# Kernel optimization log

Hardware: AMD Instinct MI355X
Metric: run time of the kernel (lower is better)

## Reference

```python
import jax, jax.numpy as jnp
import numpy as np

NUM_ITERS = 3

def squash(s, axis=-1):
    # standard capsule squash: ||s||^2/(1+||s||^2) * s/||s||
    sq = jnp.sum(s * s, axis=axis, keepdims=True)
    norm = jnp.sqrt(sq)
    return (sq / (1.0 + sq)) * (s / norm)

def setup_inputs() -> dict:
    key = jax.random.key(0)
    kx, kw = jax.random.split(key)
    B, I, k, l, O = 512, 1152, 8, 16, 7
    x = jax.random.normal(kx, (B, I, k), dtype=jnp.float32)
    w = jax.random.normal(kw, (I, k, l, O), dtype=jnp.float32)
    return {"x": x, "w": w}

def reference(x, w):
    # x: [B, I, k]; w: [I, k, l, O]
    u_hat = jnp.einsum('BIk,IklO->BIlO', x, w)            # [B, I, l, O]
    I, _, l, _ = w.shape
    b_ij = jnp.zeros((I, l), dtype=u_hat.dtype)
    v_j = None
    for _ in range(NUM_ITERS):
        c_ij = jax.nn.softmax(b_ij, axis=0)               # softmax over I
        s_j = jnp.einsum('Il,BIlO->BlO', c_ij, u_hat)     # [B, l, O]
        v_j = jnp.transpose(squash(s_j), (0, 2, 1))       # [B, O, l]
        u_vj = jnp.einsum('BOl,BIlO->BIl', v_j, u_hat).mean(axis=0)  # [I, l]
        b_ij = b_ij + u_vj
    return v_j
```

## Files before the change

### kernel.cpp

```cpp
#include <hip/hip_runtime.h>
#include <hip/hip_bf16.h>


#define NB 512
#define NI 1152
#define NLO 112
#define NIK 9216
#define NPAD 128

typedef __attribute__((ext_vector_type(8))) short bf16x8;
typedef __attribute__((ext_vector_type(4))) float f32x4;

__device__ __forceinline__ ushort f2bf(float f) {
    __hip_bfloat16 h = __float2bfloat16(f);
    return *(ushort*)&h;
}
__device__ __forceinline__ float bf2f(short s) {
    union { unsigned int u; float f; } v;
    v.u = ((unsigned int)(unsigned short)s) << 16;
    return v.f;
}

__device__ __forceinline__ void conv_x_body(const float* __restrict__ x,
                                            ushort* __restrict__ xbf,
                                            ushort* __restrict__ xT, int bid) {
    __shared__ ushort tile[64][68];
    int kg = bid % 144, bg = bid / 144;
    int k0 = kg * 64, b0 = bg * 64;
    int t = threadIdx.x;
    for (int e = t; e < 1024; e += 256) {
        int r = e >> 4, c4 = (e & 15) * 4;
        float4 f = *(const float4*)&x[(size_t)(b0 + r) * NIK + k0 + c4];
        ushort4 u = { f2bf(f.x), f2bf(f.y), f2bf(f.z), f2bf(f.w) };
        *(ushort4*)&xbf[(size_t)(b0 + r) * NIK + k0 + c4] = u;
        tile[r][c4] = u.x; tile[r][c4 + 1] = u.y; tile[r][c4 + 2] = u.z; tile[r][c4 + 3] = u.w;
    }
    __syncthreads();
    for (int e = t; e < 1024; e += 256) {
        int kr = e >> 4, c4 = (e & 15) * 4;
        ushort4 u = { tile[c4][kr], tile[c4 + 1][kr], tile[c4 + 2][kr], tile[c4 + 3][kr] };
        *(ushort4*)&xT[(size_t)(k0 + kr) * NB + b0 + c4] = u;
    }
}

__global__ __launch_bounds__(256) void prep0(const float* __restrict__ x,
                                             ushort* __restrict__ xbf,
                                             ushort* __restrict__ xT,
                                             const float* __restrict__ w,
                                             ushort* __restrict__ wpT,
                                             float* __restrict__ eb,
                                             float* __restrict__ Z) {
    if (blockIdx.x < 1152) { conv_x_body(x, xbf, xT, blockIdx.x); return; }
    __shared__ ushort tile[NPAD][66];
    int t = threadIdx.x;
    int wb = blockIdx.x - 1152;
    int ik0 = wb * 64;
    if (blockIdx.x == 1152 && t < 48) Z[t] = (t < 16) ? 1152.0f : 0.0f;
    if (t < 128) eb[(size_t)(wb * 8 + (t >> 4)) * 16 + (t & 15)] = 1.0f;
    for (int e = t; e < 8192; e += 256) {
        int ikl = e >> 7, np = e & 127;
        int l = np >> 3, o = np & 7;
        float wv = (o < 7) ? w[(size_t)(ik0 + ikl) * NLO + l * 7 + o] : 0.f;
        tile[np][ikl] = f2bf(wv);
    }
    __syncthreads();
    for (int e = t; e < 8192; e += 256) {
        int np = e >> 6, ikl = e & 63;
        wpT[(size_t)np * NIK + ik0 + ikl] = tile[np][ikl];
    }
}

__global__ __launch_bounds__(1024) void sq_gemm(const ushort* __restrict__ xbf,
                                                const ushort* __restrict__ wpT,
                                                const float* __restrict__ eb,
                                                const float* __restrict__ Zit,
                                                ushort* __restrict__ vT,
                                                float* __restrict__ out, int wout) {
    __shared__ float csl[NI * 2];
    __shared__ float sp[16][16][16];
    __shared__ float ss[16][16];
    __shared__ float facs[16][2];
    __shared__ float zi[2];
    int bid = blockIdx.x;
    int mt = bid & 31, ng = bid >> 5;
    int b0 = mt * 16, n0 = ng * 16;
    int t = threadIdx.x;
    int wv = t >> 6, lane = t & 63;
    int row = lane & 15, quad = lane >> 4;
    int k0 = wv * 576;
    for (int e = t; e < NI * 2; e += 1024) {
        int i = e >> 1, ls = e & 1;
        csl[e] = eb[(size_t)i * 16 + ng * 2 + ls];
    }
    if (t < 2) zi[t] = 1.0f / Zit[ng * 2 + t];
    __syncthreads();
    const ushort* ap = xbf + (size_t)(b0 + row) * NIK + k0 + quad * 8;
    const ushort* bp = wpT + (size_t)(n0 + row) * NIK + k0 + quad * 8;
    int lsel = row >> 3;
    int i0 = (k0 >> 3) + quad;
    f32x4 acc = {0.f, 0.f, 0.f, 0.f};
    #pragma unroll 6
    for (int ks = 0; ks < 18; ++ks) {
        bf16x8 a = *(const bf16x8*)(ap + ks * 32);
        bf16x8 wf = *(const bf16x8*)(bp + ks * 32);
        float cv = csl[(i0 + ks * 4) * 2 + lsel];
        bf16x8 b;
        #pragma unroll
        for (int j = 0; j < 8; ++j) b[j] = (short)f2bf(bf2f(wf[j]) * cv);
        acc = __builtin_amdgcn_mfma_f32_16x16x32_bf16(a, b, acc, 0, 0, 0);
    }
    #pragma unroll
    for (int r = 0; r < 4; ++r) sp[wv][quad * 4 + r][row] = acc[r];
    __syncthreads();
    if (t < 256) {
        int m = t >> 4, n = t & 15;
        float sv = 0.f;
        #pragma unroll
        for (int w8 = 0; w8 < 16; ++w8) sv += sp[w8][m][n];
        ss[m][n] = sv * zi[n >> 3];
    }
    __syncthreads();
    if (t < 32) {
        int m = t >> 1, ll = t & 1;
        float sq = 0.f;
        #pragma unroll
        for (int o = 0; o < 8; ++o) { float e = ss[m][ll * 8 + o]; sq += e * e; }
        facs[m][ll] = sqrtf(sq) / (1.0f + sq);
    }
    __syncthreads();
    if (t < 256) {
        int m = t >> 4, n = t & 15;
        int o = n & 7, lg = ng * 2 + (n >> 3);
        if (o < 7) {
            float vv = ss[m][n] * facs[m][n >> 3];
            vT[(size_t)(o * 16 + lg) * NB + b0 + m] = f2bf(vv);
            if (wout) out[(size_t)(b0 + m) * NLO + o * 16 + lg] = vv;
        }
    }
}

__global__ __launch_bounds__(512) void g_wc(const ushort* __restrict__ xT,
                                            const ushort* __restrict__ vT,
                                            const float* __restrict__ w,
                                            float* __restrict__ bij,
                                            float* __restrict__ eb,
                                            float* __restrict__ Zit, int accum) {
    __shared__ float bs[2][8][16];
    __shared__ float cs[128];
    int t = threadIdx.x;
    int wv = t >> 6;
    int lane = t & 63;
    int half = wv & 1;
    int mt = wv >> 1;
    int m0 = blockIdx.x * 64 + mt * 16;
    int kb0 = half * 256;
    int row = lane & 15, quad = lane >> 4;
    const ushort* ap = xT + (size_t)(m0 + row) * NB + kb0 + quad * 8;
    const ushort* bp = vT + (size_t)row * NB + kb0 + quad * 8;
    f32x4 acc[7];
    #pragma unroll
    for (int nt = 0; nt < 7; ++nt) acc[nt] = (f32x4){0.f, 0.f, 0.f, 0.f};
    #pragma unroll
    for (int ks = 0; ks < 8; ++ks) {
        bf16x8 a = *(const bf16x8*)(ap + ks * 32);
        #pragma unroll
        for (int nt = 0; nt < 7; ++nt) {
            bf16x8 bfr = *(const bf16x8*)(bp + (size_t)nt * 16 * NB + ks * 32);
            acc[nt] = __builtin_amdgcn_mfma_f32_16x16x32_bf16(a, bfr, acc[nt], 0, 0, 0);
        }
    }
    float S = 0.f;
    #pragma unroll
    for (int r = 0; r < 4; ++r) {
        int ik = m0 + quad * 4 + r;
        const float* wr = w + (size_t)ik * NLO + row * 7;
        float p = 0.f;
        #pragma unroll
        for (int o = 0; o < 7; ++o) p += wr[o] * acc[o][r];
        S += p;
    }
    float Sp = __shfl_down(S, 16);
    if ((quad & 1) == 0)
        bs[half][mt * 2 + (quad >> 1)][row] = (S + Sp) * (1.0f / 512.0f);
    __syncthreads();
    if (t < 128) {
        int il = t >> 4, l = t & 15;
        int i = blockIdx.x * 8 + il;
        float val = bs[0][il][l] + bs[1][il][l];
        if (accum) val += bij[i * 16 + l];
        bij[i * 16 + l] = val;
        float e = expf(val);
        cs[t] = e;
        eb[(size_t)i * 16 + l] = e;
    }
    __syncthreads();
    if (t < 16) {
        float z = 0.f;
        #pragma unroll
        for (int j = 0; j < 8; ++j) z += cs[j * 16 + t];
        atomicAdd(&Zit[t], z);
    }
}

extern "C" void kernel_launch(void* const* d_in, const int* in_sizes, int n_in,
                              void* d_out, int out_size, void* d_ws, size_t ws_size,
                              hipStream_t stream) {
    const float* x = (const float*)d_in[0];
    const float* w = (const float*)d_in[1];
    float* out = (float*)d_out;
    float* ws = (float*)d_ws;
    float*  f_bij  = ws;
    float*  f_eb   = f_bij + NI * 16;
    float*  f_Z    = f_eb + NI * 16;
    ushort* xbf    = (ushort*)(f_Z + 48);
    ushort* xT     = xbf + (size_t)NB * NIK;
    ushort* wpT    = xT + (size_t)NIK * NB;
    ushort* vT     = wpT + (size_t)NPAD * NIK;
    prep0<<<1296, 256, 0, stream>>>(x, xbf, xT, w, wpT, f_eb, f_Z);
    for (int it = 0; it < 3; ++it) {
        sq_gemm<<<256, 1024, 0, stream>>>(xbf, wpT, f_eb, f_Z + it * 16, vT, out,
                                          it == 2 ? 1 : 0);
        if (it < 2)
            g_wc<<<144, 512, 0, stream>>>(xT, vT, w, f_bij, f_eb,
                                          f_Z + (it + 1) * 16, it);
    }
}
```

Baseline: 174.9 us.

## Pre-scale weights by routing coefficients in g_wc instead of inside sq_gemm

The exp(b_ij) routing scale is now applied to the bf16 weight matrix once per iteration at the end of g_wc, which writes a scaled copy wps. sq_gemm then streams wps directly into the MFMA. This removes the per-block LDS staging of coefficients, the barrier, and the per-element bf16 multiply from the inner loop, and lets that loop unroll fully. The cost is an extra weight buffer and an extra read and write of the weight matrix per iteration, plus a duplicate write in prep0.

Result: no change. 174.1 us (-0.4%).

```diff
diff --git a/kernel.cpp b/kernel.cpp
--- a/kernel.cpp
+++ b/kernel.cpp
@@ -48,7 +48,7 @@
                                              ushort* __restrict__ xT,
                                              const float* __restrict__ w,
                                              ushort* __restrict__ wpT,
-                                             float* __restrict__ eb,
+                                             ushort* __restrict__ wps,
                                              float* __restrict__ Z) {
     if (blockIdx.x < 1152) { conv_x_body(x, xbf, xT, blockIdx.x); return; }
     __shared__ ushort tile[NPAD][66];
@@ -56,7 +56,6 @@
     int wb = blockIdx.x - 1152;
     int ik0 = wb * 64;
     if (blockIdx.x == 1152 && t < 48) Z[t] = (t < 16) ? 1152.0f : 0.0f;
-    if (t < 128) eb[(size_t)(wb * 8 + (t >> 4)) * 16 + (t & 15)] = 1.0f;
     for (int e = t; e < 8192; e += 256) {
         int ikl = e >> 7, np = e & 127;
         int l = np >> 3, o = np & 7;
@@ -66,17 +65,17 @@
     __syncthreads();
     for (int e = t; e < 8192; e += 256) {
         int np = e >> 6, ikl = e & 63;
-        wpT[(size_t)np * NIK + ik0 + ikl] = tile[np][ikl];
+        ushort v = tile[np][ikl];
+        wpT[(size_t)np * NIK + ik0 + ikl] = v;
+        wps[(size_t)np * NIK + ik0 + ikl] = v;
     }
 }
 
 __global__ __launch_bounds__(1024) void sq_gemm(const ushort* __restrict__ xbf,
-                                                const ushort* __restrict__ wpT,
-                                                const float* __restrict__ eb,
+                                                const ushort* __restrict__ wps,
                                                 const float* __restrict__ Zit,
                                                 ushort* __restrict__ vT,
                                                 float* __restrict__ out, int wout) {
-    __shared__ float csl[NI * 2];
     __shared__ float sp[16][16][16];
     __shared__ float ss[16][16];
     __shared__ float facs[16][2];
@@ -88,25 +87,14 @@
     int wv = t >> 6, lane = t & 63;
     int row = lane & 15, quad = lane >> 4;
     int k0 = wv * 576;
-    for (int e = t; e < NI * 2; e += 1024) {
-        int i = e >> 1, ls = e & 1;
-        csl[e] = eb[(size_t)i * 16 + ng * 2 + ls];
-    }
     if (t < 2) zi[t] = 1.0f / Zit[ng * 2 + t];
-    __syncthreads();
     const ushort* ap = xbf + (size_t)(b0 + row) * NIK + k0 + quad * 8;
-    const ushort* bp = wpT + (size_t)(n0 + row) * NIK + k0 + quad * 8;
-    int lsel = row >> 3;
-    int i0 = (k0 >> 3) + quad;
+    const ushort* bp = wps + (size_t)(n0 + row) * NIK + k0 + quad * 8;
     f32x4 acc = {0.f, 0.f, 0.f, 0.f};
-    #pragma unroll 6
+    #pragma unroll
     for (int ks = 0; ks < 18; ++ks) {
         bf16x8 a = *(const bf16x8*)(ap + ks * 32);
-        bf16x8 wf = *(const bf16x8*)(bp + ks * 32);
-        float cv = csl[(i0 + ks * 4) * 2 + lsel];
-        bf16x8 b;
-        #pragma unroll
-        for (int j = 0; j < 8; ++j) b[j] = (short)f2bf(bf2f(wf[j]) * cv);
+        bf16x8 b = *(const bf16x8*)(bp + ks * 32);
         acc = __builtin_amdgcn_mfma_f32_16x16x32_bf16(a, b, acc, 0, 0, 0);
     }
     #pragma unroll
@@ -143,7 +131,8 @@
                                             const ushort* __restrict__ vT,
                                             const float* __restrict__ w,
                                             float* __restrict__ bij,
-                                            float* __restrict__ eb,
+                                            const ushort* __restrict__ wpT,
+                                            ushort* __restrict__ wps,
                                             float* __restrict__ Zit, int accum) {
     __shared__ float bs[2][8][16];
     __shared__ float cs[128];
@@ -189,9 +178,7 @@
         float val = bs[0][il][l] + bs[1][il][l];
         if (accum) val += bij[i * 16 + l];
         bij[i * 16 + l] = val;
-        float e = expf(val);
-        cs[t] = e;
-        eb[(size_t)i * 16 + l] = e;
+        cs[t] = expf(val);
     }
     __syncthreads();
     if (t < 16) {
@@ -199,6 +186,15 @@
         #pragma unroll
         for (int j = 0; j < 8; ++j) z += cs[j * 16 + t];
         atomicAdd(&Zit[t], z);
+    }
+    int ik0 = blockIdx.x * 64;
+    for (int e = t; e < 2048; e += 512) {
+        int np = e >> 4, i4 = (e & 15) * 4;
+        float sc = cs[(i4 >> 3) * 16 + (np >> 3)];
+        ushort4 wv4 = *(const ushort4*)&wpT[(size_t)np * NIK + ik0 + i4];
+        ushort4 o4 = { f2bf(bf2f((short)wv4.x) * sc), f2bf(bf2f((short)wv4.y) * sc),
+                       f2bf(bf2f((short)wv4.z) * sc), f2bf(bf2f((short)wv4.w) * sc) };
+        *(ushort4*)&wps[(size_t)np * NIK + ik0 + i4] = o4;
     }
 }
 
@@ -210,18 +206,18 @@
     float* out = (float*)d_out;
     float* ws = (float*)d_ws;
     float*  f_bij  = ws;
-    float*  f_eb   = f_bij + NI * 16;
-    float*  f_Z    = f_eb + NI * 16;
+    float*  f_Z    = f_bij + NI * 16;
     ushort* xbf    = (ushort*)(f_Z + 48);
     ushort* xT     = xbf + (size_t)NB * NIK;
     ushort* wpT    = xT + (size_t)NIK * NB;
-    ushort* vT     = wpT + (size_t)NPAD * NIK;
-    prep0<<<1296, 256, 0, stream>>>(x, xbf, xT, w, wpT, f_eb, f_Z);
+    ushort* wps    = wpT + (size_t)NPAD * NIK;
+    ushort* vT     = wps + (size_t)NPAD * NIK;
+    prep0<<<1296, 256, 0, stream>>>(x, xbf, xT, w, wpT, wps, f_Z);
     for (int it = 0; it < 3; ++it) {
-        sq_gemm<<<256, 1024, 0, stream>>>(xbf, wpT, f_eb, f_Z + it * 16, vT, out,
+        sq_gemm<<<256, 1024, 0, stream>>>(xbf, wps, f_Z + it * 16, vT, out,
                                           it == 2 ? 1 : 0);
         if (it < 2)
-            g_wc<<<144, 512, 0, stream>>>(xT, vT, w, f_bij, f_eb,
+            g_wc<<<144, 512, 0, stream>>>(xT, vT, w, f_bij, wpT, wps,
                                           f_Z + (it + 1) * 16, it);
     }
 }
```

## Fuse routing iterations into one persistent kernel with grid-wide barriers

Applied to the files above, without the earlier changes.

Replaces the five alternating sq_gemm/g_wc launches with a single persistent kernel of 256 blocks. Iterations are separated by atomic-counter grid barriers, and shared data goes through agent-scope coherent loads and stores. bij is now kept in shared memory instead of global. The GEMM loop also halves the waves per block and register-prefetches six fragments ahead. This removes per-launch overhead and gaps between launches, at the cost of spin barriers that rely on all 256 blocks being co-resident, plus coherent-load overhead.

Result: slower. 466.7 us (+166.9%).

```diff
diff --git a/kernel.cpp b/kernel.cpp
--- a/kernel.cpp
+++ b/kernel.cpp
@@ -19,6 +19,35 @@
     union { unsigned int u; float f; } v;
     v.u = ((unsigned int)(unsigned short)s) << 16;
     return v.f;
+}
+
+__device__ __forceinline__ float ld_cohf(const float* p) {
+    return __hip_atomic_load((float*)p, __ATOMIC_RELAXED, __HIP_MEMORY_SCOPE_AGENT);
+}
+__device__ __forceinline__ void st_cohf(float* p, float v) {
+    __hip_atomic_store(p, v, __ATOMIC_RELAXED, __HIP_MEMORY_SCOPE_AGENT);
+}
+__device__ __forceinline__ void st_cohu(ushort* p, ushort v) {
+    __hip_atomic_store(p, v, __ATOMIC_RELAXED, __HIP_MEMORY_SCOPE_AGENT);
+}
+__device__ __forceinline__ bf16x8 ld_coh_frag(const ushort* p) {
+    union { unsigned long long q[2]; bf16x8 v; } u;
+    u.q[0] = __hip_atomic_load((unsigned long long*)p, __ATOMIC_RELAXED, __HIP_MEMORY_SCOPE_AGENT);
+    u.q[1] = __hip_atomic_load((unsigned long long*)(p + 4), __ATOMIC_RELAXED, __HIP_MEMORY_SCOPE_AGENT);
+    return u.v;
+}
+
+__device__ __forceinline__ void gbar(int* ctr, int idx) {
+    __syncthreads();
+    if (threadIdx.x == 0) {
+        asm volatile("s_waitcnt vmcnt(0)" ::: "memory");
+        __hip_atomic_fetch_add(&ctr[idx], 1, __ATOMIC_RELAXED, __HIP_MEMORY_SCOPE_AGENT);
+        while (__hip_atomic_load(&ctr[idx], __ATOMIC_RELAXED, __HIP_MEMORY_SCOPE_AGENT) < 256) {
+            __builtin_amdgcn_s_sleep(2);
+        }
+    }
+    __syncthreads();
+    __builtin_amdgcn_sched_barrier(0);
 }
 
 __device__ __forceinline__ void conv_x_body(const float* __restrict__ x,
@@ -49,13 +78,17 @@
                                              const float* __restrict__ w,
                                              ushort* __restrict__ wpT,
                                              float* __restrict__ eb,
-                                             float* __restrict__ Z) {
+                                             float* __restrict__ Z,
+                                             int* __restrict__ bar) {
     if (blockIdx.x < 1152) { conv_x_body(x, xbf, xT, blockIdx.x); return; }
     __shared__ ushort tile[NPAD][66];
     int t = threadIdx.x;
     int wb = blockIdx.x - 1152;
     int ik0 = wb * 64;
-    if (blockIdx.x == 1152 && t < 48) Z[t] = (t < 16) ? 1152.0f : 0.0f;
+    if (blockIdx.x == 1152) {
+        if (t < 48) Z[t] = (t < 16) ? 1152.0f : 0.0f;
+        if (t >= 48 && t < 64) bar[t - 48] = 0;
+    }
     if (t < 128) eb[(size_t)(wb * 8 + (t >> 4)) * 16 + (t & 15)] = 1.0f;
     for (int e = t; e < 8192; e += 256) {
         int ikl = e >> 7, np = e & 127;
@@ -70,135 +103,143 @@
     }
 }
 
-__global__ __launch_bounds__(1024) void sq_gemm(const ushort* __restrict__ xbf,
-                                                const ushort* __restrict__ wpT,
-                                                const float* __restrict__ eb,
-                                                const float* __restrict__ Zit,
-                                                ushort* __restrict__ vT,
-                                                float* __restrict__ out, int wout) {
+__global__ __launch_bounds__(512, 2) void route2(const ushort* __restrict__ xbf,
+                                                 const ushort* __restrict__ wpT,
+                                                 float* __restrict__ eb,
+                                                 float* __restrict__ Z,
+                                                 ushort* __restrict__ vT,
+                                                 float* __restrict__ out,
+                                                 const ushort* __restrict__ xT,
+                                                 const float* __restrict__ w,
+                                                 int* __restrict__ bar) {
     __shared__ float csl[NI * 2];
-    __shared__ float sp[16][16][16];
+    __shared__ float sp[8][16][16];
     __shared__ float ss[16][16];
     __shared__ float facs[16][2];
     __shared__ float zi[2];
+    __shared__ float bs[2][8][16];
+    __shared__ float cs[128];
+    __shared__ float bij_s[128];
     int bid = blockIdx.x;
-    int mt = bid & 31, ng = bid >> 5;
-    int b0 = mt * 16, n0 = ng * 16;
     int t = threadIdx.x;
     int wv = t >> 6, lane = t & 63;
     int row = lane & 15, quad = lane >> 4;
-    int k0 = wv * 576;
-    for (int e = t; e < NI * 2; e += 1024) {
-        int i = e >> 1, ls = e & 1;
-        csl[e] = eb[(size_t)i * 16 + ng * 2 + ls];
-    }
-    if (t < 2) zi[t] = 1.0f / Zit[ng * 2 + t];
-    __syncthreads();
+    int mt = bid & 31, ng = bid >> 5;
+    int b0 = mt * 16, n0 = ng * 16;
+    int k0 = wv * 1152;
+    int lsel = row >> 3;
+    int i0 = (k0 >> 3) + quad;
     const ushort* ap = xbf + (size_t)(b0 + row) * NIK + k0 + quad * 8;
     const ushort* bp = wpT + (size_t)(n0 + row) * NIK + k0 + quad * 8;
-    int lsel = row >> 3;
-    int i0 = (k0 >> 3) + quad;
-    f32x4 acc = {0.f, 0.f, 0.f, 0.f};
-    #pragma unroll 6
-    for (int ks = 0; ks < 18; ++ks) {
-        bf16x8 a = *(const bf16x8*)(ap + ks * 32);
-        bf16x8 wf = *(const bf16x8*)(bp + ks * 32);
-        float cv = csl[(i0 + ks * 4) * 2 + lsel];
-        bf16x8 b;
+
+    for (int it = 0; it < 3; ++it) {
+        for (int e = t; e < NI * 2; e += 512) {
+            int i = e >> 1, ls = e & 1;
+            csl[e] = ld_cohf(&eb[(size_t)i * 16 + ng * 2 + ls]);
+        }
+        if (t < 2) zi[t] = 1.0f / ld_cohf(&Z[it * 16 + ng * 2 + t]);
+        __syncthreads();
+        bf16x8 ab[6], wb[6];
         #pragma unroll
-        for (int j = 0; j < 8; ++j) b[j] = (short)f2bf(bf2f(wf[j]) * cv);
-        acc = __builtin_amdgcn_mfma_f32_16x16x32_bf16(a, b, acc, 0, 0, 0);
-    }
-    #pragma unroll
-    for (int r = 0; r < 4; ++r) sp[wv][quad * 4 + r][row] = acc[r];
-    __syncthreads();
-    if (t < 256) {
-        int m = t >> 4, n = t & 15;
-        float sv = 0.f;
+        for (int p = 0; p < 6; ++p) {
+            ab[p] = *(const bf16x8*)(ap + p * 32);
+            wb[p] = *(const bf16x8*)(bp + p * 32);
+        }
+        f32x4 acc = {0.f, 0.f, 0.f, 0.f};
         #pragma unroll
-        for (int w8 = 0; w8 < 16; ++w8) sv += sp[w8][m][n];
-        ss[m][n] = sv * zi[n >> 3];
-    }
-    __syncthreads();
-    if (t < 32) {
-        int m = t >> 1, ll = t & 1;
-        float sq = 0.f;
+        for (int ks = 0; ks < 36; ++ks) {
+            int s = ks % 6;
+            float cv = csl[(i0 + ks * 4) * 2 + lsel];
+            bf16x8 b;
+            #pragma unroll
+            for (int j = 0; j < 8; ++j) b[j] = (short)f2bf(bf2f(wb[s][j]) * cv);
+            acc = __builtin_amdgcn_mfma_f32_16x16x32_bf16(ab[s], b, acc, 0, 0, 0);
+            if (ks < 30) {
+                ab[s] = *(const bf16x8*)(ap + (ks + 6) * 32);
+                wb[s] = *(const bf16x8*)(bp + (ks + 6) * 32);
+            }
+        }
         #pragma unroll
-        for (int o = 0; o < 8; ++o) { float e = ss[m][ll * 8 + o]; sq += e * e; }
-        facs[m][ll] = sqrtf(sq) / (1.0f + sq);
-    }
-    __syncthreads();
-    if (t < 256) {
-        int m = t >> 4, n = t & 15;
-        int o = n & 7, lg = ng * 2 + (n >> 3);
-        if (o < 7) {
-            float vv = ss[m][n] * facs[m][n >> 3];
-            vT[(size_t)(o * 16 + lg) * NB + b0 + m] = f2bf(vv);
-            if (wout) out[(size_t)(b0 + m) * NLO + o * 16 + lg] = vv;
-        }
-    }
-}
-
-__global__ __launch_bounds__(512) void g_wc(const ushort* __restrict__ xT,
-                                            const ushort* __restrict__ vT,
-                                            const float* __restrict__ w,
-                                            float* __restrict__ bij,
-                                            float* __restrict__ eb,
-                                            float* __restrict__ Zit, int accum) {
-    __shared__ float bs[2][8][16];
-    __shared__ float cs[128];
-    int t = threadIdx.x;
-    int wv = t >> 6;
-    int lane = t & 63;
-    int half = wv & 1;
-    int mt = wv >> 1;
-    int m0 = blockIdx.x * 64 + mt * 16;
-    int kb0 = half * 256;
-    int row = lane & 15, quad = lane >> 4;
-    const ushort* ap = xT + (size_t)(m0 + row) * NB + kb0 + quad * 8;
-    const ushort* bp = vT + (size_t)row * NB + kb0 + quad * 8;
-    f32x4 acc[7];
-    #pragma unroll
-    for (int nt = 0; nt < 7; ++nt) acc[nt] = (f32x4){0.f, 0.f, 0.f, 0.f};
-    #pragma unroll
-    for (int ks = 0; ks < 8; ++ks) {
-        bf16x8 a = *(const bf16x8*)(ap + ks * 32);
-        #pragma unroll
-        for (int nt = 0; nt < 7; ++nt) {
-            bf16x8 bfr = *(const bf16x8*)(bp + (size_t)nt * 16 * NB + ks * 32);
-            acc[nt] = __builtin_amdgcn_mfma_f32_16x16x32_bf16(a, bfr, acc[nt], 0, 0, 0);
-        }
-    }
-    float S = 0.f;
-    #pragma unroll
-    for (int r = 0; r < 4; ++r) {
-        int ik = m0 + quad * 4 + r;
-        const float* wr = w + (size_t)ik * NLO + row * 7;
-        float p = 0.f;
-        #pragma unroll
-        for (int o = 0; o < 7; ++o) p += wr[o] * acc[o][r];
-        S += p;
-    }
-    float Sp = __shfl_down(S, 16);
-    if ((quad & 1) == 0)
-        bs[half][mt * 2 + (quad >> 1)][row] = (S + Sp) * (1.0f / 512.0f);
-    __syncthreads();
-    if (t < 128) {
-        int il = t >> 4, l = t & 15;
-        int i = blockIdx.x * 8 + il;
-        float val = bs[0][il][l] + bs[1][il][l];
-        if (accum) val += bij[i * 16 + l];
-        bij[i * 16 + l] = val;
-        float e = expf(val);
-        cs[t] = e;
-        eb[(size_t)i * 16 + l] = e;
-    }
-    __syncthreads();
-    if (t < 16) {
-        float z = 0.f;
-        #pragma unroll
-        for (int j = 0; j < 8; ++j) z += cs[j * 16 + t];
-        atomicAdd(&Zit[t], z);
+        for (int r = 0; r < 4; ++r) sp[wv][quad * 4 + r][row] = acc[r];
+        __syncthreads();
+        if (t < 256) {
+            int m = t >> 4, n = t & 15;
+            float sv = 0.f;
+            #pragma unroll
+            for (int w8 = 0; w8 < 8; ++w8) sv += sp[w8][m][n];
+            ss[m][n] = sv * zi[n >> 3];
+        }
+        __syncthreads();
+        if (t < 32) {
+            int m = t >> 1, ll = t & 1;
+            float sq = 0.f;
+            #pragma unroll
+            for (int o = 0; o < 8; ++o) { float e = ss[m][ll * 8 + o]; sq += e * e; }
+            facs[m][ll] = sqrtf(sq) / (1.0f + sq);
+        }
+        __syncthreads();
+        if (t < 256) {
+            int m = t >> 4, n = t & 15;
+            int o = n & 7, lg = ng * 2 + (n >> 3);
+            if (o < 7) {
+                float vv = ss[m][n] * facs[m][n >> 3];
+                st_cohu(&vT[(size_t)(o * 16 + lg) * NB + b0 + m], f2bf(vv));
+                if (it == 2) out[(size_t)(b0 + m) * NLO + o * 16 + lg] = vv;
+            }
+        }
+        if (it == 2) break;
+        gbar(bar, 2 * it);
+
+        if (bid < 144) {
+            int half = wv & 1;
+            int mtg = wv >> 1;
+            int m0 = bid * 64 + mtg * 16;
+            int kb0 = half * 256;
+            const ushort* gap = xT + (size_t)(m0 + row) * NB + kb0 + quad * 8;
+            const ushort* gbp = vT + (size_t)row * NB + kb0 + quad * 8;
+            f32x4 gacc[7];
+            #pragma unroll
+            for (int nt = 0; nt < 7; ++nt) gacc[nt] = (f32x4){0.f, 0.f, 0.f, 0.f};
+            for (int ks = 0; ks < 8; ++ks) {
+                bf16x8 a = *(const bf16x8*)(gap + ks * 32);
+                #pragma unroll
+                for (int nt = 0; nt < 7; ++nt) {
+                    bf16x8 bfr = ld_coh_frag(gbp + (size_t)nt * 16 * NB + ks * 32);
+                    gacc[nt] = __builtin_amdgcn_mfma_f32_16x16x32_bf16(a, bfr, gacc[nt], 0, 0, 0);
+                }
+            }
+            float S = 0.f;
+            #pragma unroll
+            for (int r = 0; r < 4; ++r) {
+                int ik = m0 + quad * 4 + r;
+                const float* wr = w + (size_t)ik * NLO + row * 7;
+                float p = 0.f;
+                #pragma unroll
+                for (int o = 0; o < 7; ++o) p += wr[o] * gacc[o][r];
+                S += p;
+            }
+            float Sp = __shfl_down(S, 16);
+            if ((quad & 1) == 0)
+                bs[half][mtg * 2 + (quad >> 1)][row] = (S + Sp) * (1.0f / 512.0f);
+            __syncthreads();
+            if (t < 128) {
+                float val = bs[0][t >> 4][t & 15] + bs[1][t >> 4][t & 15];
+                if (it) val += bij_s[t];
+                bij_s[t] = val;
+                float e = expf(val);
+                cs[t] = e;
+                int i = bid * 8 + (t >> 4);
+                st_cohf(&eb[(size_t)i * 16 + (t & 15)], e);
+            }
+            __syncthreads();
+            if (t < 16) {
+                float z = 0.f;
+                #pragma unroll
+                for (int j = 0; j < 8; ++j) z += cs[j * 16 + t];
+                atomicAdd(&Z[(it + 1) * 16 + t], z);
+            }
+        }
+        gbar(bar, 2 * it + 1);
     }
 }
 
@@ -209,19 +250,13 @@
     const float* w = (const float*)d_in[1];
     float* out = (float*)d_out;
     float* ws = (float*)d_ws;
-    float*  f_bij  = ws;
-    float*  f_eb   = f_bij + NI * 16;
-    float*  f_Z    = f_eb + NI * 16;
-    ushort* xbf    = (ushort*)(f_Z + 48);
+    float*  f_Z    = ws;
+    int*    bar    = (int*)(ws + 48);
+    float*  f_eb   = ws + 64;
+    ushort* xbf    = (ushort*)(f_eb + NI * 16);
     ushort* xT     = xbf + (size_t)NB * NIK;
     ushort* wpT    = xT + (size_t)NIK * NB;
     ushort* vT     = wpT + (size_t)NPAD * NIK;
-    prep0<<<1296, 256, 0, stream>>>(x, xbf, xT, w, wpT, f_eb, f_Z);
-    for (int it = 0; it < 3; ++it) {
-        sq_gemm<<<256, 1024, 0, stream>>>(xbf, wpT, f_eb, f_Z + it * 16, vT, out,
-                                          it == 2 ? 1 : 0);
-        if (it < 2)
-            g_wc<<<144, 512, 0, stream>>>(xT, vT, w, f_bij, f_eb,
-                                          f_Z + (it + 1) * 16, it);
-    }
-}
+    prep0<<<1296, 256, 0, stream>>>(x, xbf, xT, w, wpT, f_eb, f_Z, bar);
+    route2<<<256, 512, 0, stream>>>(xbf, wpT, f_eb, f_Z, vT, out, xT, w, bar);
+}
```

## Fuse agreement update into squash GEMM kernel and compute softmax normalizer in-block

Applied to the files above, without the earlier changes.

Removes the separate g_wc kernel: each sqg block now computes its own v slice and immediately multiplies it against xT and w to atomically accumulate the agreement update into b_ij. The exp and softmax normalizer are computed inside each block from b_ij rather than from precomputed exp buffers and a global Z, and block size drops from 1024 to 512 threads with a longer K loop. This cuts launches and removes the vT round trip, in exchange for many float atomics, redundant exp/reduction per block, and less parallelism in the main GEMM loop.

Measured after the change: 296.1 us. +69.3%, slower.

```diff
diff --git a/kernel.cpp b/kernel.cpp
--- a/kernel.cpp
+++ b/kernel.cpp
@@ -48,15 +48,17 @@
                                              ushort* __restrict__ xT,
                                              const float* __restrict__ w,
                                              ushort* __restrict__ wpT,
-                                             float* __restrict__ eb,
-                                             float* __restrict__ Z) {
+                                             float* __restrict__ bij0,
+                                             float* __restrict__ bij1) {
     if (blockIdx.x < 1152) { conv_x_body(x, xbf, xT, blockIdx.x); return; }
     __shared__ ushort tile[NPAD][66];
     int t = threadIdx.x;
     int wb = blockIdx.x - 1152;
     int ik0 = wb * 64;
-    if (blockIdx.x == 1152 && t < 48) Z[t] = (t < 16) ? 1152.0f : 0.0f;
-    if (t < 128) eb[(size_t)(wb * 8 + (t >> 4)) * 16 + (t & 15)] = 1.0f;
+    if (t < 128) {
+        bij0[wb * 128 + t] = 0.f;
+        bij1[wb * 128 + t] = 0.f;
+    }
     for (int e = t; e < 8192; e += 256) {
         int ikl = e >> 7, np = e & 127;
         int l = np >> 3, o = np & 7;
@@ -70,40 +72,59 @@
     }
 }
 
-__global__ __launch_bounds__(1024) void sq_gemm(const ushort* __restrict__ xbf,
-                                                const ushort* __restrict__ wpT,
-                                                const float* __restrict__ eb,
-                                                const float* __restrict__ Zit,
-                                                ushort* __restrict__ vT,
-                                                float* __restrict__ out, int wout) {
+__global__ __launch_bounds__(512, 2) void sqg(const ushort* __restrict__ xbf,
+                                              const ushort* __restrict__ xT,
+                                              const ushort* __restrict__ wpT,
+                                              const float* __restrict__ w,
+                                              const float* __restrict__ bijA,
+                                              float* __restrict__ bijW,
+                                              float* __restrict__ out, int it) {
     __shared__ float csl[NI * 2];
-    __shared__ float sp[16][16][16];
+    __shared__ float sp[8][16][16];
     __shared__ float ss[16][16];
     __shared__ float facs[16][2];
-    __shared__ float zi[2];
+    __shared__ float zp[512];
+    __shared__ float zfin[2];
     int bid = blockIdx.x;
-    int mt = bid & 31, ng = bid >> 5;
-    int b0 = mt * 16, n0 = ng * 16;
     int t = threadIdx.x;
     int wv = t >> 6, lane = t & 63;
     int row = lane & 15, quad = lane >> 4;
-    int k0 = wv * 576;
-    for (int e = t; e < NI * 2; e += 1024) {
-        int i = e >> 1, ls = e & 1;
-        csl[e] = eb[(size_t)i * 16 + ng * 2 + ls];
-    }
-    if (t < 2) zi[t] = 1.0f / Zit[ng * 2 + t];
-    __syncthreads();
+    int mt = bid & 31, ng = bid >> 5;
+    int b0 = mt * 16, n0 = ng * 16;
+    int k0 = wv * 1152;
+    int lsel = row >> 3;
+
+    float zacc = 0.f;
+    if (it == 0) {
+        for (int e = t; e < NI * 2; e += 512) csl[e] = 1.0f;
+    } else {
+        for (int e = t; e < NI * 2; e += 512) {
+            int i = e >> 1, lg = ng * 2 + (e & 1);
+            float v = bijA[i * 16 + lg];
+            if (it == 2) v += bijW[i * 16 + lg];
+            float c = expf(v);
+            csl[e] = c; zacc += c;
+        }
+    }
+    zp[t] = zacc;
+    __syncthreads();
+    #pragma unroll
+    for (int s = 256; s >= 2; s >>= 1) {
+        if (t < s) zp[t] += zp[t + s];
+        __syncthreads();
+    }
+    if (t < 2) zfin[t] = (it == 0) ? (1.0f / 1152.0f) : 1.0f / zp[t];
+    __syncthreads();
+
     const ushort* ap = xbf + (size_t)(b0 + row) * NIK + k0 + quad * 8;
     const ushort* bp = wpT + (size_t)(n0 + row) * NIK + k0 + quad * 8;
-    int lsel = row >> 3;
-    int i0 = (k0 >> 3) + quad;
+    int ibase = 144 * wv + quad;
     f32x4 acc = {0.f, 0.f, 0.f, 0.f};
     #pragma unroll 6
-    for (int ks = 0; ks < 18; ++ks) {
+    for (int ks = 0; ks < 36; ++ks) {
         bf16x8 a = *(const bf16x8*)(ap + ks * 32);
         bf16x8 wf = *(const bf16x8*)(bp + ks * 32);
-        float cv = csl[(i0 + ks * 4) * 2 + lsel];
+        float cv = csl[(ibase + ks * 4) * 2 + lsel];
         bf16x8 b;
         #pragma unroll
         for (int j = 0; j < 8; ++j) b[j] = (short)f2bf(bf2f(wf[j]) * cv);
@@ -116,8 +137,8 @@
         int m = t >> 4, n = t & 15;
         float sv = 0.f;
         #pragma unroll
-        for (int w8 = 0; w8 < 16; ++w8) sv += sp[w8][m][n];
-        ss[m][n] = sv * zi[n >> 3];
+        for (int w8 = 0; w8 < 8; ++w8) sv += sp[w8][m][n];
+        ss[m][n] = sv * zfin[n >> 3];
     }
     __syncthreads();
     if (t < 32) {
@@ -128,77 +149,57 @@
         facs[m][ll] = sqrtf(sq) / (1.0f + sq);
     }
     __syncthreads();
-    if (t < 256) {
-        int m = t >> 4, n = t & 15;
-        int o = n & 7, lg = ng * 2 + (n >> 3);
-        if (o < 7) {
-            float vv = ss[m][n] * facs[m][n >> 3];
-            vT[(size_t)(o * 16 + lg) * NB + b0 + m] = f2bf(vv);
-            if (wout) out[(size_t)(b0 + m) * NLO + o * 16 + lg] = vv;
-        }
-    }
-}
-
-__global__ __launch_bounds__(512) void g_wc(const ushort* __restrict__ xT,
-                                            const ushort* __restrict__ vT,
-                                            const float* __restrict__ w,
-                                            float* __restrict__ bij,
-                                            float* __restrict__ eb,
-                                            float* __restrict__ Zit, int accum) {
-    __shared__ float bs[2][8][16];
-    __shared__ float cs[128];
-    int t = threadIdx.x;
-    int wv = t >> 6;
-    int lane = t & 63;
-    int half = wv & 1;
-    int mt = wv >> 1;
-    int m0 = blockIdx.x * 64 + mt * 16;
-    int kb0 = half * 256;
-    int row = lane & 15, quad = lane >> 4;
-    const ushort* ap = xT + (size_t)(m0 + row) * NB + kb0 + quad * 8;
-    const ushort* bp = vT + (size_t)row * NB + kb0 + quad * 8;
-    f32x4 acc[7];
-    #pragma unroll
-    for (int nt = 0; nt < 7; ++nt) acc[nt] = (f32x4){0.f, 0.f, 0.f, 0.f};
-    #pragma unroll
-    for (int ks = 0; ks < 8; ++ks) {
-        bf16x8 a = *(const bf16x8*)(ap + ks * 32);
-        #pragma unroll
-        for (int nt = 0; nt < 7; ++nt) {
-            bf16x8 bfr = *(const bf16x8*)(bp + (size_t)nt * 16 * NB + ks * 32);
-            acc[nt] = __builtin_amdgcn_mfma_f32_16x16x32_bf16(a, bfr, acc[nt], 0, 0, 0);
-        }
-    }
-    float S = 0.f;
-    #pragma unroll
-    for (int r = 0; r < 4; ++r) {
-        int ik = m0 + quad * 4 + r;
-        const float* wr = w + (size_t)ik * NLO + row * 7;
+
+    if (it == 2) {
+        if (t < 256) {
+            int m = t >> 4, n = t & 15;
+            int o = n & 7, lg = ng * 2 + (n >> 3);
+            if (o < 7)
+                out[(size_t)(b0 + m) * NLO + o * 16 + lg] = ss[m][n] * facs[m][n >> 3];
+        }
+        return;
+    }
+
+    int o2 = row & 7, ls2 = lsel;
+    bf16x8 bfv;
+    if (quad < 2) {
+        #pragma unroll
+        for (int j = 0; j < 8; ++j) {
+            int bl = quad * 8 + j;
+            float vv = (o2 == 7) ? 0.f : ss[bl][row] * facs[bl][ls2];
+            bfv[j] = (short)f2bf(vv);
+        }
+    } else {
+        #pragma unroll
+        for (int j = 0; j < 8; ++j) bfv[j] = 0;
+    }
+    const float* wbase = w + (size_t)0 * NLO + (ng * 2 + ls2) * 7 + o2;
+    f32x4 zero4 = {0.f, 0.f, 0.f, 0.f};
+    int rep = ((quad & 1) == 0) && (o2 == 0);
+    int lg2 = ng * 2 + ls2;
+    for (int j = 0; j < 72; ++j) {
+        int tl = wv * 72 + j;
+        int ik0t = tl * 16;
+        bf16x8 af;
+        if (quad < 2)
+            af = *(const bf16x8*)(xT + (size_t)(ik0t + row) * NB + b0 + quad * 8);
+        else {
+            #pragma unroll
+            for (int q = 0; q < 8; ++q) af[q] = 0;
+        }
+        f32x4 g = __builtin_amdgcn_mfma_f32_16x16x32_bf16(af, bfv, zero4, 0, 0, 0);
         float p = 0.f;
-        #pragma unroll
-        for (int o = 0; o < 7; ++o) p += wr[o] * acc[o][r];
-        S += p;
-    }
-    float Sp = __shfl_down(S, 16);
-    if ((quad & 1) == 0)
-        bs[half][mt * 2 + (quad >> 1)][row] = (S + Sp) * (1.0f / 512.0f);
-    __syncthreads();
-    if (t < 128) {
-        int il = t >> 4, l = t & 15;
-        int i = blockIdx.x * 8 + il;
-        float val = bs[0][il][l] + bs[1][il][l];
-        if (accum) val += bij[i * 16 + l];
-        bij[i * 16 + l] = val;
-        float e = expf(val);
-        cs[t] = e;
-        eb[(size_t)i * 16 + l] = e;
-    }
-    __syncthreads();
-    if (t < 16) {
-        float z = 0.f;
-        #pragma unroll
-        for (int j = 0; j < 8; ++j) z += cs[j * 16 + t];
-        atomicAdd(&Zit[t], z);
+        if (o2 < 7) {
+            const float* wr = wbase + (size_t)(ik0t + quad * 4) * NLO;
+            #pragma unroll
+            for (int r = 0; r < 4; ++r) p += g[r] * wr[(size_t)r * NLO];
+        }
+        p += __shfl_xor(p, 16);
+        p += __shfl_xor(p, 1);
+        p += __shfl_xor(p, 2);
+        p += __shfl_xor(p, 4);
+        if (rep)
+            atomicAdd(&bijW[(tl * 2 + (quad >> 1)) * 16 + lg2], p * (1.0f / 512.0f));
     }
 }
 
@@ -209,19 +210,13 @@
     const float* w = (const float*)d_in[1];
     float* out = (float*)d_out;
     float* ws = (float*)d_ws;
-    float*  f_bij  = ws;
-    float*  f_eb   = f_bij + NI * 16;
-    float*  f_Z    = f_eb + NI * 16;
-    ushort* xbf    = (ushort*)(f_Z + 48);
-    ushort* xT     = xbf + (size_t)NB * NIK;
-    ushort* wpT    = xT + (size_t)NIK * NB;
-    ushort* vT     = wpT + (size_t)NPAD * NIK;
-    prep0<<<1296, 256, 0, stream>>>(x, xbf, xT, w, wpT, f_eb, f_Z);
-    for (int it = 0; it < 3; ++it) {
-        sq_gemm<<<256, 1024, 0, stream>>>(xbf, wpT, f_eb, f_Z + it * 16, vT, out,
-                                          it == 2 ? 1 : 0);
-        if (it < 2)
-            g_wc<<<144, 512, 0, stream>>>(xT, vT, w, f_bij, f_eb,
-                                          f_Z + (it + 1) * 16, it);
-    }
-}
+    float*  bij0 = ws;
+    float*  bij1 = bij0 + NI * 16;
+    ushort* xbf  = (ushort*)(bij1 + NI * 16);
+    ushort* xT   = xbf + (size_t)NB * NIK;
+    ushort* wpT  = xT + (size_t)NIK * NB;
+    prep0<<<1296, 256, 0, stream>>>(x, xbf, xT, w, wpT, bij0, bij1);
+    sqg<<<256, 512, 0, stream>>>(xbf, xT, wpT, w, bij1, bij0, out, 0);
+    sqg<<<256, 512, 0, stream>>>(xbf, xT, wpT, w, bij0, bij1, out, 1);
+    sqg<<<256, 512, 0, stream>>>(xbf, xT, wpT, w, bij0, bij1, out, 2);
+}
```
